# Kernel optimization log

Measured on AMD Instinct MI355X. Metric: run time of the kernel, lower is better.

The kernel has to match this reference:

```python
import jax, jax.numpy as jnp
import numpy as np

B = 256          # number of enclosing subgraphs (one candidate link each)
N_PER = 128      # nodes per subgraph (== max_nodes)
N = B * N_PER
DEG = 8
E_REAL = N * DEG
E = E_REAL + 2 * B
H = 32           # hidden_channels
HEADS = 2
WALK_LEN = 7
MAX_Z = 1000
L = 3            # num_layers
LRELU = 0.2


def setup_inputs() -> dict:
    rng = np.random.default_rng(0)
    goff = (np.arange(B) * N_PER)[:, None]
    # real edges: random sources, tiled targets so every node has >=1 incoming edge
    lr = rng.integers(0, N_PER, size=(B, N_PER * DEG))
    lc = np.broadcast_to(np.tile(np.arange(N_PER), DEG), (B, N_PER * DEG))
    row_real = (lr + goff).reshape(-1)
    col_real = (lc + goff).reshape(-1)
    # one candidate link (i,j) per graph, stored as interleaved (i->j, j->i)
    i_loc = rng.integers(0, N_PER, size=B)
    j_loc = (i_loc + 1 + rng.integers(0, N_PER - 1, size=B)) % N_PER
    node_i = i_loc + np.arange(B) * N_PER
    node_j = j_loc + np.arange(B) * N_PER
    cand_row = np.stack([node_i, node_j], 1).reshape(-1)
    cand_col = np.stack([node_j, node_i], 1).reshape(-1)
    key = jax.random.key(0)
    ks = jax.random.split(key, 10)
    s = 0.05
    return dict(
        z_table=jax.random.normal(ks[1], (MAX_Z, H)) * s,
        conv_W=jax.random.normal(ks[2], (L, H, H)) * s,
        conv_b=jnp.zeros((L, H)),
        k1_W=jax.random.normal(ks[3], (H, H)) * s, k1_b=jnp.zeros((H,)),
        q1_W=jax.random.normal(ks[4], (H, H)) * s, q1_b=jnp.zeros((H,)),
        k2_W=jax.random.normal(ks[5], (H, HEADS * H)) * s, k2_b=jnp.zeros((HEADS * H,)),
        q2_W=jax.random.normal(ks[6], (H, HEADS * H)) * s, q2_b=jnp.zeros((HEADS * H,)),
        mlp_W1=jax.random.normal(ks[7], (WALK_LEN * HEADS * 5 + HEADS, H)) * s,
        mlp_b1=jnp.zeros((H,)),
        mlp_W2=jax.random.normal(ks[8], (H, 1)) * s,
        mlp_b2=jnp.zeros((1,)),
        z=jax.random.randint(ks[0], (N,), 0, MAX_Z, dtype=jnp.int32),
        edge_row=jnp.asarray(np.concatenate([row_real, cand_row]), jnp.int32),
        edge_col=jnp.asarray(np.concatenate([col_real, cand_col]), jnp.int32),
        edge_mask=jnp.asarray(np.concatenate([np.ones(E_REAL, bool), np.zeros(2 * B, bool)])),
        batch=jnp.repeat(jnp.arange(B, dtype=jnp.int32), N_PER),
        node_i=jnp.asarray(node_i, jnp.int32),
        node_j=jnp.asarray(node_j, jnp.int32),
    )


def _forward(z_table, conv_W, conv_b, k1_W, k1_b, q1_W, q1_b, k2_W, k2_b, q2_W, q2_b,
             mlp_W1, mlp_b1, mlp_W2, mlp_b2,
             z, edge_row, edge_col, edge_mask, batch, node_i, node_j):
    # ---- GCN stack (eval mode: dropout / dropedge are identity) ----
    x = z_table[z]                                    # (N, H)
    loops = jnp.arange(N, dtype=edge_row.dtype)
    row2 = jnp.concatenate([edge_row, loops])         # add self loops
    col2 = jnp.concatenate([edge_col, loops])
    deg = jax.ops.segment_sum(jnp.ones_like(col2, x.dtype), col2, N)
    dinv = jax.lax.rsqrt(deg)                         # deg >= 1 due to self loops
    gnorm = dinv[row2] * dinv[col2]
    for l in range(L):
        xw = x @ conv_W[l]
        x = jax.ops.segment_sum(gnorm[:, None] * xw[row2], col2, N) + conv_b[l]
        if l < L - 1:
            x = jax.nn.relu(x)
    # ---- WalkPooling attention weights ----
    q = jax.nn.leaky_relu(x @ k1_W + k1_b, LRELU)
    k = jax.nn.leaky_relu(x @ q1_W + q1_b, LRELU)
    q = (q @ k2_W + k2_b).reshape(N, HEADS, H)
    k = (k @ q2_W + q2_b).reshape(N, HEADS, H)
    w = jnp.sum(q[edge_row] * k[edge_col], -1) / np.sqrt(H)   # (E, HEADS)
    wmax = jax.ops.segment_max(w, edge_col, N)
    ew = jnp.exp(w - wmax[edge_col])
    weights_p = ew / (jax.ops.segment_sum(ew, edge_col, N)[edge_col] + 1e-16)
    ewm = ew * edge_mask[:, None]                     # candidate link removed
    weights_m = ewm / (jax.ops.segment_sum(ewm, edge_col, N)[edge_col] + 1e-16)
    # omega: scores at the 2B candidate edges (stored last), summed per pair
    wc = jax.nn.sigmoid(w[E_REAL:])                   # (2B, HEADS)
    omega = wc[1::2] + wc[0::2]                       # (B, HEADS)
    # local node index within each graph
    arangeN = jnp.arange(N, dtype=jnp.int32)
    starts = jax.ops.segment_min(arangeN, batch, B)
    index = arangeN - starts[batch]                   # (N,)
    idx_i = index[node_i]
    idx_j = index[node_j]
    x0 = jnp.zeros((N, N_PER), x.dtype).at[arangeN, index].set(1.0)
    x0 = jnp.broadcast_to(x0, (HEADS, N, N_PER))

    def propagate(xh, wcol):                          # xh (HEADS,N,M), wcol (E,HEADS)
        def one(xi, wi):
            return jax.ops.segment_sum(wi[:, None] * xi[edge_row], edge_col, N)
        return jax.vmap(one, in_axes=(0, 1))(xh, wcol)

    xp = propagate(x0, weights_p)
    xm = propagate(x0, weights_m)

    def feats(xh):
        nl = xh[:, node_i, idx_i] + xh[:, node_j, idx_j]   # (HEADS, B)
        ll = xh[:, node_i, idx_j] + xh[:, node_j, idx_i]
        diag = xh[:, arangeN, index]                        # (HEADS, N)
        g = jax.vmap(lambda d: jax.ops.segment_sum(d, batch, B))(diag)
        return nl, ll, g

    def step(carry, _):
        xp, xm = carry
        xp = propagate(xp, weights_p)
        xm = propagate(xm, weights_m)
        nlp, llp, gp = feats(xp)
        nlm, llm, gm = feats(xm)
        return (xp, xm), (nlp, nlm, llp, llm, gp - gm)

    _, (nlp, nlm, llp, llm, gl) = jax.lax.scan(step, (xp, xm), None, length=WALK_LEN)

    def to_feat(a):                                    # (WALK_LEN,HEADS,B) -> (B, HEADS*WALK_LEN)
        return jnp.transpose(a, (2, 1, 0)).reshape(B, HEADS * WALK_LEN)

    feat = jnp.concatenate([to_feat(gl), omega, to_feat(nlp), to_feat(nlm),
                            to_feat(llp), to_feat(llm)], axis=1)   # (B, 72)
    h1 = jax.nn.relu(feat @ mlp_W1 + mlp_b1)
    return h1 @ mlp_W2 + mlp_b2                        # (B, 1)


def reference(z_table, conv_W, conv_b, k1_W, k1_b, q1_W, q1_b, k2_W, k2_b, q2_W, q2_b,
              mlp_W1, mlp_b1, mlp_W2, mlp_b2,
              z, edge_row, edge_col, edge_mask, batch, node_i, node_j):
    return _forward(z_table, conv_W, conv_b, k1_W, k1_b, q1_W, q1_b, k2_W, k2_b,
                    q2_W, q2_b, mlp_W1, mlp_b1, mlp_W2, mlp_b2,
                    z, edge_row, edge_col, edge_mask, batch, node_i, node_j)
```

## Files before the change

### kernel.cpp

```cpp
#include <hip/hip_runtime.h>

#define NB 256
#define NPER 128
#define NN 32768
#define DEG 8
#define EREAL (NN*DEG)
#define HH 32
#define NHEADS 2
#define WLEN 7
#define RSQRT_H 0.17677669529663687f

#define FRONT_LDS 136208
#define WALK2_LDS 139520

__device__ __forceinline__ int sidx8(int n, int v){
    return n*128 + ((((v>>2) ^ (n&31))<<2) | (v&3));
}

__global__ __launch_bounds__(1024) void k_front(
    const float* __restrict__ z_table, const int* __restrict__ z,
    const float* __restrict__ convW, const float* __restrict__ convb,
    const float* __restrict__ k1W, const float* __restrict__ k1b,
    const float* __restrict__ q1W, const float* __restrict__ q1b,
    const float* __restrict__ k2W, const float* __restrict__ k2b,
    const float* __restrict__ q2W, const float* __restrict__ q2b,
    const int* __restrict__ erow, const int* __restrict__ node_i, const int* __restrict__ node_j,
    float2* __restrict__ wp8, float* __restrict__ rat_g,
    float* __restrict__ exw_g, float* __restrict__ omega_g)
{
    extern __shared__ char sm[];
    float* xl   = (float*)sm;
    float* t1   = (float*)(sm + 16384);
    float* t2   = (float*)(sm + 32768);
    float* Wb   = (float*)(sm + 49152);
    float* rowf = (float*)(sm + 65536);
    float* colf = (float*)(sm + 98304);
    int*   rows = (int*)(sm + 131072);
    float* dinv = (float*)(sm + 135168);
    float* bias = (float*)(sm + 135680);
    float* omg  = (float*)(sm + 136192);

    int b = blockIdx.x, tid = threadIdx.x;
    int iloc = node_i[b] & 127, jloc = node_j[b] & 127;

    #pragma unroll
    for (int ii=0;ii<4;ii++){
        int i = tid + ii*1024;
        int n = i>>5, d = i&31;
        xl[i] = z_table[z[b*128+n]*32 + d];
    }
    rows[(tid&127)*8 + (tid>>7)] = erow[b*1024 + tid] & 127;
    if (tid < 128) dinv[tid] = rsqrtf((tid==iloc||tid==jloc)? 10.f : 9.f);

    int j = tid & 31, rg = tid>>5;
    for (int l=0;l<3;l++){
        __syncthreads();
        Wb[tid] = convW[l*1024+tid];
        if (tid<32) bias[tid] = convb[l*32+tid];
        __syncthreads();
        float Wc[32];
        #pragma unroll
        for (int k=0;k<32;k++) Wc[k] = Wb[k*32+j];
        #pragma unroll
        for (int ii=0;ii<4;ii++){
            int r = rg + 32*ii;
            const float4* xr = (const float4*)&xl[r*32];
            float a = 0.f;
            #pragma unroll
            for (int k4=0;k4<8;k4++){
                float4 xv = xr[k4];
                a += xv.x*Wc[4*k4] + xv.y*Wc[4*k4+1] + xv.z*Wc[4*k4+2] + xv.w*Wc[4*k4+3];
            }
            t1[r*32+j] = a;
        }
        __syncthreads();
        #pragma unroll
        for (int ii=0;ii<4;ii++){
            int c = rg + 32*ii;
            float acc = dinv[c]*t1[c*32+j];
            #pragma unroll
            for (int s=0;s<8;s++){
                int r = rows[c*8+s];
                acc += dinv[r]*t1[r*32+j];
            }
            if (c==iloc) acc += dinv[jloc]*t1[jloc*32+j];
            if (c==jloc) acc += dinv[iloc]*t1[iloc*32+j];
            float v = dinv[c]*acc + bias[j];
            if (l<2) v = fmaxf(v,0.f);
            xl[c*32+j] = v;
        }
    }
    __syncthreads();
    for (int i=tid;i<2048;i+=1024) Wb[i] = (i<1024)? k1W[i] : q1W[i-1024];
    if (tid<64) bias[tid] = (tid<32)? k1b[tid] : q1b[tid-32];
    __syncthreads();
    {
        float Wa[32], Wq[32];
        #pragma unroll
        for (int k=0;k<32;k++){ Wa[k] = Wb[k*32+j]; Wq[k] = Wb[1024 + k*32+j]; }
        #pragma unroll
        for (int ii=0;ii<4;ii++){
            int n = rg + 32*ii;
            const float4* xr = (const float4*)&xl[n*32];
            float a1 = bias[j], a2 = bias[32+j];
            #pragma unroll
            for (int k4=0;k4<8;k4++){
                float4 xv = xr[k4];
                a1 += xv.x*Wa[4*k4] + xv.y*Wa[4*k4+1] + xv.z*Wa[4*k4+2] + xv.w*Wa[4*k4+3];
                a2 += xv.x*Wq[4*k4] + xv.y*Wq[4*k4+1] + xv.z*Wq[4*k4+2] + xv.w*Wq[4*k4+3];
            }
            t1[n*32+j] = a1>0.f? a1 : 0.2f*a1;
            t2[n*32+j] = a2>0.f? a2 : 0.2f*a2;
        }
    }
    __syncthreads();
    for (int i=tid;i<4096;i+=1024) Wb[i] = (i<2048)? k2W[i] : q2W[i-2048];
    if (tid<128) bias[tid] = (tid<64)? k2b[tid] : q2b[tid-64];
    __syncthreads();
    {
        int j2 = tid & 63, rg2 = tid>>6;
        float Wk[32], Wq[32];
        #pragma unroll
        for (int k=0;k<32;k++){ Wk[k] = Wb[k*64+j2]; Wq[k] = Wb[2048 + k*64+j2]; }
        #pragma unroll
        for (int ii=0;ii<8;ii++){
            int n = rg2 + 16*ii;
            const float4* u4 = (const float4*)&t1[n*32];
            const float4* v4 = (const float4*)&t2[n*32];
            float o1 = bias[j2], o2 = bias[64+j2];
            #pragma unroll
            for (int k4=0;k4<8;k4++){
                float4 u = u4[k4], v = v4[k4];
                o1 += u.x*Wk[4*k4] + u.y*Wk[4*k4+1] + u.z*Wk[4*k4+2] + u.w*Wk[4*k4+3];
                o2 += v.x*Wq[4*k4] + v.y*Wq[4*k4+1] + v.z*Wq[4*k4+2] + v.w*Wq[4*k4+3];
            }
            int sidx = n*64 + ((((j2>>2) ^ (n&7)) << 2) | (j2&3));
            rowf[sidx] = o1;
            colf[sidx] = o2;
        }
    }
    float* warr = Wb;
    __syncthreads();
    {
        int c = tid & 127, h = (tid>>7)&1, sgrp = tid>>8;
        int cs = c&7, h8 = h*8;
        const float4* cf = (const float4*)&colf[c*64];
        float4 kv[8];
        #pragma unroll
        for (int k4=0;k4<8;k4++) kv[k4] = cf[h8 + (k4^cs)];
        #pragma unroll
        for (int si=0;si<2;si++){
            int s = sgrp*2+si;
            int r = rows[c*8+s];
            int rs = r&7;
            const float4* rf = (const float4*)&rowf[r*64];
            float a = 0.f;
            #pragma unroll
            for (int k4=0;k4<8;k4++){
                float4 q = rf[h8 + (k4^rs)];
                a += q.x*kv[k4].x + q.y*kv[k4].y + q.z*kv[k4].z + q.w*kv[k4].w;
            }
            warr[(h*128+c)*9+s] = a*RSQRT_H;
        }
        if (sgrp==0){
            int r = -1;
            if (c==jloc) r = iloc; else if (c==iloc) r = jloc;
            float a = -3.0e38f;
            if (r>=0){
                int rs = r&7;
                const float4* rf = (const float4*)&rowf[r*64];
                a = 0.f;
                #pragma unroll
                for (int k4=0;k4<8;k4++){
                    float4 q = rf[h8 + (k4^rs)];
                    a += q.x*kv[k4].x + q.y*kv[k4].y + q.z*kv[k4].z + q.w*kv[k4].w;
                }
                a *= RSQRT_H;
            }
            warr[(h*128+c)*9+8] = a;
        }
    }
    __syncthreads();
    if (tid < 256){
        int c = tid & 127, h = tid >> 7;
        float wv[9];
        #pragma unroll
        for (int s=0;s<9;s++) wv[s] = warr[(h*128+c)*9+s];
        float wmax = wv[0];
        #pragma unroll
        for (int s=1;s<9;s++) wmax = fmaxf(wmax, wv[s]);
        float e[9]; float sp = 0.f;
        #pragma unroll
        for (int s=0;s<9;s++){ e[s] = expf(wv[s]-wmax); sp += e[s]; }
        float sm_ = sp - e[8];
        float rp = 1.f/(sp+1e-16f);
        float rat = (sp+1e-16f)/(sm_+1e-16f);
        size_t base = ((size_t)h*NN + b*128 + c)*8;
        #pragma unroll
        for (int s=0;s<8;s++)
            wp8[base+s] = make_float2(e[s]*rp, __int_as_float(rows[c*8+s]));
        rat_g[h*NN + b*128 + c] = rat;
        if (c==jloc || c==iloc){
            int k = (c==jloc)? 0 : 1;
            exw_g[(b*2+h)*2 + k] = e[8]*rp;
            omg[h*2+k] = 1.f/(1.f+expf(-wv[8]));
        }
    }
    __syncthreads();
    if (tid < 2) omega_g[b*2+tid] = omg[tid*2] + omg[tid*2+1];
}

__global__ __launch_bounds__(1024) void k_walk(
    const float2* __restrict__ wp8, const float* __restrict__ rat_g,
    const float* __restrict__ exw_g,
    const int* __restrict__ node_i, const int* __restrict__ node_j,
    float* __restrict__ featbuf)
{
    extern __shared__ char sm[];
    float*  PX = (float*)sm;
    float*  PY = (float*)(sm + 65536);
    float*  cwT= (float*)(sm + 131072);
    int*    crT= (int*)  (sm + 135168);
    float*  scr= (float*)(sm + 139264);
    int bid = blockIdx.x;
    int b = bid>>2, h = (bid>>1)&1, sg = bid&1;
    int tid = threadIdx.x;

    {   float2 p = wp8[((size_t)h*NN + b*128)*8 + tid];
        if (sg) p.x *= rat_g[h*NN + b*128 + (tid>>3)];
        cwT[(tid&7)*128 + (tid>>3)] = p.x;
        crT[(tid&7)*128 + (tid>>3)] = __float_as_int(p.y);
    }
    int iloc = node_i[b]&127, jloc = node_j[b]&127;
    float exw0=0.f, exw1=0.f; int exc0=-1, exc1=-1;
    if (!sg){
        exw0 = exw_g[(b*2+h)*2+0];
        exw1 = exw_g[(b*2+h)*2+1];
        exc0 = jloc; exc1 = iloc;
    }
    {   float4* PX4 = (float4*)PX;
        #pragma unroll
        for (int k=0;k<4;k++) PX4[tid + k*1024] = make_float4(0.f,0.f,0.f,0.f);
    }
    __syncthreads();
    if (tid >= 64 && tid < 192){
        int c = tid - 64;
        #pragma unroll
        for (int s=0;s<8;s++){
            float w = cwT[s*128+c];
            int   r = crT[s*128+c];
            PX[sidx8(c, r)] += w;
        }
        if (c==exc0) PX[sidx8(c, iloc)] += exw0;
        if (c==exc1) PX[sidx8(c, jloc)] += exw1;
    }
    if (tid < 64){
        int l = tid;
        float ci0 = (iloc==l)?1.f:0.f, ci1 = (iloc==64+l)?1.f:0.f;
        float cj0 = (jloc==l)?1.f:0.f, cj1 = (jloc==64+l)?1.f:0.f;
        int il = iloc&63, jl = jloc&63;
        for (int t=1;t<=9;t++){
            float a0 = __shfl(ci0, il), a1 = __shfl(ci1, il);
            float b0 = __shfl(cj0, il), b1 = __shfl(cj1, il);
            float c0 = __shfl(ci0, jl), c1 = __shfl(ci1, jl);
            float d0 = __shfl(cj0, jl), d1 = __shfl(cj1, jl);
            float vi_ci = (iloc<64)? a0:a1;
            float vi_cj = (iloc<64)? b0:b1;
            float vj_ci = (jloc<64)? c0:c1;
            float vj_cj = (jloc<64)? d0:d1;
            if (t>=3 && l==0){
                int tt = t-3;
                featbuf[((0*2+sg)*WLEN + tt)*(NHEADS*NB) + h*NB + b] = vi_ci + vj_cj;
                featbuf[((1*2+sg)*WLEN + tt)*(NHEADS*NB) + h*NB + b] = vi_cj + vj_ci;
            }
            if (t<=8){
                float nci0=0.f,ncj0=0.f,nci1=0.f,ncj1=0.f;
                #pragma unroll
                for (int s=0;s<8;s++){
                    float w0 = cwT[s*128+l];   int r0 = crT[s*128+l];
                    float xlo = __shfl(ci0, r0&63), xhi = __shfl(ci1, r0&63);
                    float ylo = __shfl(cj0, r0&63), yhi = __shfl(cj1, r0&63);
                    nci0 += w0 * ((r0<64)? xlo:xhi);
                    ncj0 += w0 * ((r0<64)? ylo:yhi);
                    float w1 = cwT[s*128+64+l]; int r1 = crT[s*128+64+l];
                    xlo = __shfl(ci0, r1&63); xhi = __shfl(ci1, r1&63);
                    ylo = __shfl(cj0, r1&63); yhi = __shfl(cj1, r1&63);
                    nci1 += w1 * ((r1<64)? xlo:xhi);
                    ncj1 += w1 * ((r1<64)? ylo:yhi);
                }
                if (exc0==l)    { nci0 += exw0*vi_ci; ncj0 += exw0*vi_cj; }
                if (exc0==64+l) { nci1 += exw0*vi_ci; ncj1 += exw0*vi_cj; }
                if (exc1==l)    { nci0 += exw1*vj_ci; ncj0 += exw1*vj_cj; }
                if (exc1==64+l) { nci1 += exw1*vj_ci; ncj1 += exw1*vj_cj; }
                ci0=nci0; ci1=nci1; cj0=ncj0; cj1=ncj1;
            }
        }
    }
    __syncthreads();

    int c = tid>>3, j8 = tid&7, cx = c&31;
    int jj = j8 ^ (c&7);
    auto mult = [&](float* dst, const float* src){
        float4 a0={0,0,0,0}, a1={0,0,0,0}, a2={0,0,0,0}, a3={0,0,0,0};
        #pragma unroll
        for (int s=0;s<8;s++){
            float w = cwT[s*128+c];
            int   r = crT[s*128+c];
            const float4* srow = (const float4*)src + r*32;
            int rx = r&31;
            float4 v0=srow[(jj+ 0)^rx], v1=srow[(jj+ 8)^rx], v2=srow[(jj+16)^rx], v3=srow[(jj+24)^rx];
            a0.x+=w*v0.x; a0.y+=w*v0.y; a0.z+=w*v0.z; a0.w+=w*v0.w;
            a1.x+=w*v1.x; a1.y+=w*v1.y; a1.z+=w*v1.z; a1.w+=w*v1.w;
            a2.x+=w*v2.x; a2.y+=w*v2.y; a2.z+=w*v2.z; a2.w+=w*v2.w;
            a3.x+=w*v3.x; a3.y+=w*v3.y; a3.z+=w*v3.z; a3.w+=w*v3.w;
        }
        if (c==exc0){
            const float4* srow = (const float4*)src + iloc*32; int rx = iloc&31;
            float4 v0=srow[(jj+ 0)^rx], v1=srow[(jj+ 8)^rx], v2=srow[(jj+16)^rx], v3=srow[(jj+24)^rx];
            a0.x+=exw0*v0.x; a0.y+=exw0*v0.y; a0.z+=exw0*v0.z; a0.w+=exw0*v0.w;
            a1.x+=exw0*v1.x; a1.y+=exw0*v1.y; a1.z+=exw0*v1.z; a1.w+=exw0*v1.w;
            a2.x+=exw0*v2.x; a2.y+=exw0*v2.y; a2.z+=exw0*v2.z; a2.w+=exw0*v2.w;
            a3.x+=exw0*v3.x; a3.y+=exw0*v3.y; a3.z+=exw0*v3.z; a3.w+=exw0*v3.w;
        }
        if (c==exc1){
            const float4* srow = (const float4*)src + jloc*32; int rx = jloc&31;
            float4 v0=srow[(jj+ 0)^rx], v1=srow[(jj+ 8)^rx], v2=srow[(jj+16)^rx], v3=srow[(jj+24)^rx];
            a0.x+=exw1*v0.x; a0.y+=exw1*v0.y; a0.z+=exw1*v0.z; a0.w+=exw1*v0.w;
            a1.x+=exw1*v1.x; a1.y+=exw1*v1.y; a1.z+=exw1*v1.z; a1.w+=exw1*v1.w;
            a2.x+=exw1*v2.x; a2.y+=exw1*v2.y; a2.z+=exw1*v2.z; a2.w+=exw1*v2.w;
            a3.x+=exw1*v3.x; a3.y+=exw1*v3.y; a3.z+=exw1*v3.z; a3.w+=exw1*v3.w;
        }
        float4* drow = (float4*)dst + c*32;
        drow[(jj+ 0)^cx]=a0; drow[(jj+ 8)^cx]=a1; drow[(jj+16)^cx]=a2; drow[(jj+24)^cx]=a3;
    };
    auto wreduce = [](float v){
        #pragma unroll
        for (int o=32;o;o>>=1) v += __shfl_down(v,o);
        return v;
    };

    mult(PY, PX);
    __syncthreads();
    mult(PX, PY);
    if (tid<128){
        float d = wreduce(PY[sidx8(tid,tid)]);
        if ((tid&63)==0) scr[0+(tid>>6)] = d;
    }
    __syncthreads();
    mult(PY, PX);
    if (tid<128){
        float d = wreduce(PX[sidx8(tid,tid)]);
        if ((tid&63)==0) scr[2+(tid>>6)] = d;
    }
    __syncthreads();
    if (tid<128){
        float d = wreduce(PY[sidx8(tid,tid)]);
        if ((tid&63)==0) scr[4+(tid>>6)] = d;
        float s5 = 0.f;
        #pragma unroll
        for (int s=0;s<8;s++){
            float w = cwT[s*128+tid];
            int   r = crT[s*128+tid];
            s5 += w * PY[sidx8(r, tid)];
        }
        if (tid==exc0) s5 += exw0 * PY[sidx8(iloc, jloc)];
        if (tid==exc1) s5 += exw1 * PY[sidx8(jloc, iloc)];
        s5 = wreduce(s5);
        if ((tid&63)==0) scr[6+(tid>>6)] = s5;
    }
    {
        float t6=0.f, t7=0.f, t8=0.f;
        #pragma unroll
        for (int m=0;m<16;m++){
            int bb = j8 + 8*m;
            int ai = sidx8(c, bb);
            int bi = sidx8(bb, c);
            float a3 = PX[ai], a4 = PY[ai];
            float b3 = PX[bi], b4 = PY[bi];
            t6 += a3*b3; t7 += a3*b4; t8 += a4*b4;
        }
        t6 = wreduce(t6); t7 = wreduce(t7); t8 = wreduce(t8);
        int w = tid>>6;
        if ((tid&63)==0){ scr[8+w]=t6; scr[24+w]=t7; scr[40+w]=t8; }
    }
    __syncthreads();
    if (tid==0){
        float tr2=scr[0]+scr[1], tr3=scr[2]+scr[3], tr4=scr[4]+scr[5], tr5=scr[6]+scr[7];
        float t6=0.f,t7=0.f,t8=0.f;
        #pragma unroll
        for (int w=0;w<16;w++){ t6+=scr[8+w]; t7+=scr[24+w]; t8+=scr[40+w]; }
        int gb = ((2*2+sg)*WLEN)*(NHEADS*NB) + h*NB + b;
        featbuf[gb+0*(NHEADS*NB)] = tr2;
        featbuf[gb+1*(NHEADS*NB)] = tr3;
        featbuf[gb+2*(NHEADS*NB)] = tr4;
        featbuf[gb+3*(NHEADS*NB)] = tr5;
        featbuf[gb+4*(NHEADS*NB)] = t6;
        featbuf[gb+5*(NHEADS*NB)] = t7;
        featbuf[gb+6*(NHEADS*NB)] = t8;
    }
}

__global__ __launch_bounds__(256) void k_final(const float* __restrict__ W1, const float* __restrict__ b1,
                       const float* __restrict__ W2, const float* __restrict__ b2,
                       const float* __restrict__ featbuf, const float* __restrict__ omega,
                       float* __restrict__ out){
    __shared__ float sW1[72*HH];
    __shared__ float sb1[HH];
    __shared__ float sW2[HH];
    __shared__ float sb2;
    int tid = threadIdx.x;
    for (int i=tid;i<72*HH;i+=256) sW1[i] = W1[i];
    if (tid<HH){ sb1[tid]=b1[tid]; sW2[tid]=W2[tid]; }
    if (tid==0) sb2 = b2[0];
    __syncthreads();
    int b = tid;
    float h1[HH];
    #pragma unroll
    for (int j2=0;j2<HH;j2++) h1[j2] = sb1[j2];
    auto rd = [&](int idx){ return featbuf[idx]; };
    auto addf = [&](int fi, float v){
        #pragma unroll
        for (int j2=0;j2<HH;j2++) h1[j2] += v * sW1[fi*HH + j2];
    };
    for (int h2=0;h2<NHEADS;h2++)
        for (int t=0;t<WLEN;t++){
            float gp = rd(((2*2+0)*WLEN+t)*(NHEADS*NB)+h2*NB+b);
            float gm = rd(((2*2+1)*WLEN+t)*(NHEADS*NB)+h2*NB+b);
            addf(h2*WLEN+t, gp-gm);
        }
    for (int h2=0;h2<NHEADS;h2++) addf(14+h2, omega[b*NHEADS+h2]);
    for (int h2=0;h2<NHEADS;h2++)
        for (int t=0;t<WLEN;t++){
            addf(16+h2*WLEN+t, rd(((0*2+0)*WLEN+t)*(NHEADS*NB)+h2*NB+b));
            addf(30+h2*WLEN+t, rd(((0*2+1)*WLEN+t)*(NHEADS*NB)+h2*NB+b));
            addf(44+h2*WLEN+t, rd(((1*2+0)*WLEN+t)*(NHEADS*NB)+h2*NB+b));
            addf(58+h2*WLEN+t, rd(((1*2+1)*WLEN+t)*(NHEADS*NB)+h2*NB+b));
        }
    float o = sb2;
    #pragma unroll
    for (int j2=0;j2<HH;j2++) o += fmaxf(h1[j2],0.f)*sW2[j2];
    out[b] = o;
}

extern "C" void kernel_launch(void* const* d_in, const int* in_sizes, int n_in,
                              void* d_out, int out_size, void* d_ws, size_t ws_size,
                              hipStream_t stream){
    const float* z_table = (const float*)d_in[0];
    const float* convW   = (const float*)d_in[1];
    const float* convb   = (const float*)d_in[2];
    const float* k1W     = (const float*)d_in[3];
    const float* k1b     = (const float*)d_in[4];
    const float* q1W     = (const float*)d_in[5];
    const float* q1b     = (const float*)d_in[6];
    const float* k2W     = (const float*)d_in[7];
    const float* k2b     = (const float*)d_in[8];
    const float* q2W     = (const float*)d_in[9];
    const float* q2b     = (const float*)d_in[10];
    const float* mW1     = (const float*)d_in[11];
    const float* mb1     = (const float*)d_in[12];
    const float* mW2     = (const float*)d_in[13];
    const float* mb2     = (const float*)d_in[14];
    const int* z         = (const int*)d_in[15];
    const int* erow      = (const int*)d_in[16];
    const int* node_i    = (const int*)d_in[20];
    const int* node_j    = (const int*)d_in[21];
    float* out = (float*)d_out;

    char* ws = (char*)d_ws;
    size_t off = 0;
    auto alloc = [&](size_t bytes){ void* p = ws + off; off += (bytes + 255) & ~255ULL; return p; };
    float2* wp8     = (float2*)alloc((size_t)NHEADS*NN*8*8);
    float*  rat     = (float*) alloc((size_t)NHEADS*NN*4);
    float*  exw     = (float*) alloc((size_t)NB*NHEADS*2*4);
    float*  omega   = (float*) alloc((size_t)NB*NHEADS*4);
    float*  featbuf = (float*) alloc((size_t)3*2*WLEN*NHEADS*NB*4);

    hipFuncSetAttribute((const void*)k_front, hipFuncAttributeMaxDynamicSharedMemorySize, FRONT_LDS);
    hipFuncSetAttribute((const void*)k_walk,  hipFuncAttributeMaxDynamicSharedMemorySize, WALK2_LDS);

    k_front<<<NB,   1024, FRONT_LDS, stream>>>(z_table, z, convW, convb,
                                               k1W,k1b,q1W,q1b,k2W,k2b,q2W,q2b,
                                               erow, node_i, node_j, wp8, rat, exw, omega);
    k_walk <<<NB*4, 1024, WALK2_LDS, stream>>>(wp8, rat, exw, node_i, node_j, featbuf);
    k_final<<<1,    256,  0,         stream>>>(mW1, mb1, mW2, mb2, featbuf, omega, out);
}
```

Measured before the change: 216.3 us.

## Use single in-place LDS matrix buffer in walk kernel to halve shared memory

The walk kernel now keeps one 128x128 matrix in LDS instead of ping-ponging between two. Each product is accumulated in registers, and the block synchronises before writing back in place. The t6/t7/t8 trace features are recomputed from the register accumulators and the single buffer, so the second buffer is no longer needed. Dropping LDS per block from about 139KB to 74KB is meant to let two 1024-thread blocks share a CU. The cost is extra barriers and higher register pressure from holding the accumulators across phases.

Measured after the change: 209.5 us. -3.2%, faster.

```diff
diff --git a/kernel.cpp b/kernel.cpp
--- a/kernel.cpp
+++ b/kernel.cpp
@@ -11,7 +11,7 @@
 #define RSQRT_H 0.17677669529663687f
 
 #define FRONT_LDS 136208
-#define WALK2_LDS 139520
+#define WALK3_LDS 73984
 
 __device__ __forceinline__ int sidx8(int n, int v){
     return n*128 + ((((v>>2) ^ (n&31))<<2) | (v&3));
@@ -210,18 +210,17 @@
     if (tid < 2) omega_g[b*2+tid] = omg[tid*2] + omg[tid*2+1];
 }
 
-__global__ __launch_bounds__(1024) void k_walk(
+__global__ __launch_bounds__(1024, 8) void k_walk(
     const float2* __restrict__ wp8, const float* __restrict__ rat_g,
     const float* __restrict__ exw_g,
     const int* __restrict__ node_i, const int* __restrict__ node_j,
     float* __restrict__ featbuf)
 {
     extern __shared__ char sm[];
-    float*  PX = (float*)sm;
-    float*  PY = (float*)(sm + 65536);
-    float*  cwT= (float*)(sm + 131072);
-    int*    crT= (int*)  (sm + 135168);
-    float*  scr= (float*)(sm + 139264);
+    float*  PM = (float*)sm;
+    float*  cwT= (float*)(sm + 65536);
+    int*    crT= (int*)  (sm + 69632);
+    float*  scr= (float*)(sm + 73728);
     int bid = blockIdx.x;
     int b = bid>>2, h = (bid>>1)&1, sg = bid&1;
     int tid = threadIdx.x;
@@ -238,9 +237,9 @@
         exw1 = exw_g[(b*2+h)*2+1];
         exc0 = jloc; exc1 = iloc;
     }
-    {   float4* PX4 = (float4*)PX;
-        #pragma unroll
-        for (int k=0;k<4;k++) PX4[tid + k*1024] = make_float4(0.f,0.f,0.f,0.f);
+    {   float4* PM4 = (float4*)PM;
+        #pragma unroll
+        for (int k=0;k<4;k++) PM4[tid + k*1024] = make_float4(0.f,0.f,0.f,0.f);
     }
     __syncthreads();
     if (tid >= 64 && tid < 192){
@@ -249,10 +248,10 @@
         for (int s=0;s<8;s++){
             float w = cwT[s*128+c];
             int   r = crT[s*128+c];
-            PX[sidx8(c, r)] += w;
-        }
-        if (c==exc0) PX[sidx8(c, iloc)] += exw0;
-        if (c==exc1) PX[sidx8(c, jloc)] += exw1;
+            PM[sidx8(c, r)] += w;
+        }
+        if (c==exc0) PM[sidx8(c, iloc)] += exw0;
+        if (c==exc1) PM[sidx8(c, jloc)] += exw1;
     }
     if (tid < 64){
         int l = tid;
@@ -300,13 +299,14 @@
 
     int c = tid>>3, j8 = tid&7, cx = c&31;
     int jj = j8 ^ (c&7);
-    auto mult = [&](float* dst, const float* src){
-        float4 a0={0,0,0,0}, a1={0,0,0,0}, a2={0,0,0,0}, a3={0,0,0,0};
+    float4 a0,a1,a2,a3;
+    auto macc = [&](){
+        a0=make_float4(0,0,0,0); a1=a0; a2=a0; a3=a0;
         #pragma unroll
         for (int s=0;s<8;s++){
             float w = cwT[s*128+c];
             int   r = crT[s*128+c];
-            const float4* srow = (const float4*)src + r*32;
+            const float4* srow = (const float4*)PM + r*32;
             int rx = r&31;
             float4 v0=srow[(jj+ 0)^rx], v1=srow[(jj+ 8)^rx], v2=srow[(jj+16)^rx], v3=srow[(jj+24)^rx];
             a0.x+=w*v0.x; a0.y+=w*v0.y; a0.z+=w*v0.z; a0.w+=w*v0.w;
@@ -315,7 +315,7 @@
             a3.x+=w*v3.x; a3.y+=w*v3.y; a3.z+=w*v3.z; a3.w+=w*v3.w;
         }
         if (c==exc0){
-            const float4* srow = (const float4*)src + iloc*32; int rx = iloc&31;
+            const float4* srow = (const float4*)PM + iloc*32; int rx = iloc&31;
             float4 v0=srow[(jj+ 0)^rx], v1=srow[(jj+ 8)^rx], v2=srow[(jj+16)^rx], v3=srow[(jj+24)^rx];
             a0.x+=exw0*v0.x; a0.y+=exw0*v0.y; a0.z+=exw0*v0.z; a0.w+=exw0*v0.w;
             a1.x+=exw0*v1.x; a1.y+=exw0*v1.y; a1.z+=exw0*v1.z; a1.w+=exw0*v1.w;
@@ -323,14 +323,16 @@
             a3.x+=exw0*v3.x; a3.y+=exw0*v3.y; a3.z+=exw0*v3.z; a3.w+=exw0*v3.w;
         }
         if (c==exc1){
-            const float4* srow = (const float4*)src + jloc*32; int rx = jloc&31;
+            const float4* srow = (const float4*)PM + jloc*32; int rx = jloc&31;
             float4 v0=srow[(jj+ 0)^rx], v1=srow[(jj+ 8)^rx], v2=srow[(jj+16)^rx], v3=srow[(jj+24)^rx];
             a0.x+=exw1*v0.x; a0.y+=exw1*v0.y; a0.z+=exw1*v0.z; a0.w+=exw1*v0.w;
             a1.x+=exw1*v1.x; a1.y+=exw1*v1.y; a1.z+=exw1*v1.z; a1.w+=exw1*v1.w;
             a2.x+=exw1*v2.x; a2.y+=exw1*v2.y; a2.z+=exw1*v2.z; a2.w+=exw1*v2.w;
             a3.x+=exw1*v3.x; a3.y+=exw1*v3.y; a3.z+=exw1*v3.z; a3.w+=exw1*v3.w;
         }
-        float4* drow = (float4*)dst + c*32;
+    };
+    auto wrt = [&](){
+        float4* drow = (float4*)PM + c*32;
         drow[(jj+ 0)^cx]=a0; drow[(jj+ 8)^cx]=a1; drow[(jj+16)^cx]=a2; drow[(jj+24)^cx]=a3;
     };
     auto wreduce = [](float v){
@@ -338,57 +340,81 @@
         for (int o=32;o;o>>=1) v += __shfl_down(v,o);
         return v;
     };
-
-    mult(PY, PX);
-    __syncthreads();
-    mult(PX, PY);
+    int w = tid>>6;
+
+    macc();
+    __syncthreads();
+    wrt();
+    __syncthreads();
+    macc();
     if (tid<128){
-        float d = wreduce(PY[sidx8(tid,tid)]);
+        float d = wreduce(PM[sidx8(tid,tid)]);
         if ((tid&63)==0) scr[0+(tid>>6)] = d;
     }
     __syncthreads();
-    mult(PY, PX);
+    wrt();
+    __syncthreads();
+    macc();
     if (tid<128){
-        float d = wreduce(PX[sidx8(tid,tid)]);
+        float d = wreduce(PM[sidx8(tid,tid)]);
         if ((tid&63)==0) scr[2+(tid>>6)] = d;
     }
+    {
+        float t6=0.f;
+        #pragma unroll
+        for (int m=0;m<16;m++){
+            int bb = j8 + 8*m;
+            t6 += PM[sidx8(c, bb)] * PM[sidx8(bb, c)];
+        }
+        t6 = wreduce(t6);
+        if ((tid&63)==0) scr[8+w] = t6;
+    }
+    {
+        float t7=0.f;
+        #pragma unroll
+        for (int e=0;e<4;e++){
+            t7 += ((const float*)&a0)[e] * PM[sidx8(4*(jj   )+e, c)];
+            t7 += ((const float*)&a1)[e] * PM[sidx8(4*(jj+ 8)+e, c)];
+            t7 += ((const float*)&a2)[e] * PM[sidx8(4*(jj+16)+e, c)];
+            t7 += ((const float*)&a3)[e] * PM[sidx8(4*(jj+24)+e, c)];
+        }
+        t7 = wreduce(t7);
+        if ((tid&63)==0) scr[24+w] = t7;
+    }
+    __syncthreads();
+    wrt();
     __syncthreads();
     if (tid<128){
-        float d = wreduce(PY[sidx8(tid,tid)]);
+        float d = wreduce(PM[sidx8(tid,tid)]);
         if ((tid&63)==0) scr[4+(tid>>6)] = d;
         float s5 = 0.f;
         #pragma unroll
         for (int s=0;s<8;s++){
-            float w = cwT[s*128+tid];
-            int   r = crT[s*128+tid];
-            s5 += w * PY[sidx8(r, tid)];
-        }
-        if (tid==exc0) s5 += exw0 * PY[sidx8(iloc, jloc)];
-        if (tid==exc1) s5 += exw1 * PY[sidx8(jloc, iloc)];
+            float ww = cwT[s*128+tid];
+            int   r  = crT[s*128+tid];
+            s5 += ww * PM[sidx8(r, tid)];
+        }
+        if (tid==exc0) s5 += exw0 * PM[sidx8(iloc, jloc)];
+        if (tid==exc1) s5 += exw1 * PM[sidx8(jloc, iloc)];
         s5 = wreduce(s5);
         if ((tid&63)==0) scr[6+(tid>>6)] = s5;
     }
     {
-        float t6=0.f, t7=0.f, t8=0.f;
+        float t8=0.f;
         #pragma unroll
         for (int m=0;m<16;m++){
             int bb = j8 + 8*m;
-            int ai = sidx8(c, bb);
-            int bi = sidx8(bb, c);
-            float a3 = PX[ai], a4 = PY[ai];
-            float b3 = PX[bi], b4 = PY[bi];
-            t6 += a3*b3; t7 += a3*b4; t8 += a4*b4;
-        }
-        t6 = wreduce(t6); t7 = wreduce(t7); t8 = wreduce(t8);
-        int w = tid>>6;
-        if ((tid&63)==0){ scr[8+w]=t6; scr[24+w]=t7; scr[40+w]=t8; }
+            t8 += PM[sidx8(c, bb)] * PM[sidx8(bb, c)];
+        }
+        t8 = wreduce(t8);
+        if ((tid&63)==0) scr[40+w] = t8;
     }
     __syncthreads();
     if (tid==0){
         float tr2=scr[0]+scr[1], tr3=scr[2]+scr[3], tr4=scr[4]+scr[5], tr5=scr[6]+scr[7];
         float t6=0.f,t7=0.f,t8=0.f;
         #pragma unroll
-        for (int w=0;w<16;w++){ t6+=scr[8+w]; t7+=scr[24+w]; t8+=scr[40+w]; }
+        for (int k=0;k<16;k++){ t6+=scr[8+k]; t7+=scr[24+k]; t8+=scr[40+k]; }
         int gb = ((2*2+sg)*WLEN)*(NHEADS*NB) + h*NB + b;
         featbuf[gb+0*(NHEADS*NB)] = tr2;
         featbuf[gb+1*(NHEADS*NB)] = tr3;
@@ -476,11 +502,11 @@
     float*  featbuf = (float*) alloc((size_t)3*2*WLEN*NHEADS*NB*4);
 
     hipFuncSetAttribute((const void*)k_front, hipFuncAttributeMaxDynamicSharedMemorySize, FRONT_LDS);
-    hipFuncSetAttribute((const void*)k_walk,  hipFuncAttributeMaxDynamicSharedMemorySize, WALK2_LDS);
+    hipFuncSetAttribute((const void*)k_walk,  hipFuncAttributeMaxDynamicSharedMemorySize, WALK3_LDS);
 
     k_front<<<NB,   1024, FRONT_LDS, stream>>>(z_table, z, convW, convb,
                                                k1W,k1b,q1W,q1b,k2W,k2b,q2W,q2b,
                                                erow, node_i, node_j, wp8, rat, exw, omega);
-    k_walk <<<NB*4, 1024, WALK2_LDS, stream>>>(wp8, rat, exw, node_i, node_j, featbuf);
+    k_walk <<<NB*4, 1024, WALK3_LDS, stream>>>(wp8, rat, exw, node_i, node_j, featbuf);
     k_final<<<1,    256,  0,         stream>>>(mW1, mb1, mW2, mb2, featbuf, omega, out);
 }
```
